# Optimization experiments

Measured on AMD Instinct MI355X. Metric: run time of the kernel, lower is better.

## Reference

```python
import jax, jax.numpy as jnp
import numpy as np

B, N, K, C, NH = 2, 16384, 16, 256, 4
HD = C // NH  # head_dim = 64


def knn_gather(feat, idx):
    # feat: [B, N, D], idx: [B, N, K] -> [B, N, K, D]
    b, n, k = idx.shape
    d = feat.shape[-1]
    flat = jnp.take_along_axis(feat, idx.reshape(b, n * k)[..., None], axis=1)
    return flat.reshape(b, n, k, d)


def setup_inputs() -> dict:
    key = jax.random.key(0)
    ks = jax.random.split(key, 16)
    s_c = 1.0 / np.sqrt(C)
    s_4 = 1.0 / np.sqrt(4.0)
    s_hd = 1.0 / np.sqrt(HD)
    return {
        'h': jax.random.normal(ks[0], (B, N, C), jnp.float32),
        'P': jax.random.normal(ks[1], (B, 3, N), jnp.float32),
        'idx': jax.random.randint(ks[2], (B, N, K), 0, N),
        'Wq': jax.random.normal(ks[3], (C, C), jnp.float32) * s_c,
        'Wk': jax.random.normal(ks[4], (C, C), jnp.float32) * s_c,
        'Wv': jax.random.normal(ks[5], (C, C), jnp.float32) * s_c,
        'Wp1': jax.random.normal(ks[6], (4, C), jnp.float32) * s_4,
        'bp1': jnp.zeros((C,), jnp.float32),
        'Wp2': jax.random.normal(ks[7], (C, C), jnp.float32) * s_c,
        'bp2': jnp.zeros((C,), jnp.float32),
        'Wa1': jax.random.normal(ks[8], (HD, HD), jnp.float32) * s_hd,
        'ba1': jnp.zeros((HD,), jnp.float32),
        'Wa2': jax.random.normal(ks[9], (HD, 1), jnp.float32) * s_hd,
        'ba2': jnp.zeros((1,), jnp.float32),
        'Wo': jax.random.normal(ks[10], (C, C), jnp.float32) * s_c,
        'bo': jnp.zeros((C,), jnp.float32),
    }


def reference(h, P, idx, Wq, Wk, Wv, Wp1, bp1, Wp2, bp2, Wa1, ba1, Wa2, ba2, Wo, bo):
    b, n, c = h.shape
    P_t = jnp.swapaxes(P, 1, 2)                       # [B, N, 3]
    P_nbr = knn_gather(P_t, idx)                      # [B, N, K, 3]
    rel_pos = P_nbr - P_t[:, :, None, :]              # [B, N, K, 3]
    dist = jnp.linalg.norm(rel_pos, axis=-1, keepdims=True)
    geom = jnp.concatenate([rel_pos, dist], axis=-1)  # [B, N, K, 4]
    pe = jax.nn.relu(geom @ Wp1 + bp1) @ Wp2 + bp2    # [B, N, K, C]
    pe = pe.reshape(b, n, K, NH, HD)

    Q = (h @ Wq).reshape(b, n, 1, NH, HD)
    K_nbr = knn_gather(h @ Wk, idx).reshape(b, n, K, NH, HD)
    V_nbr = knn_gather(h @ Wv, idx).reshape(b, n, K, NH, HD)

    relation = Q - K_nbr + pe                          # [B, N, K, NH, HD]
    logits = jax.nn.relu(relation @ Wa1 + ba1) @ Wa2 + ba2  # [B, N, K, NH, 1]
    attn = jax.nn.softmax(logits, axis=2)              # softmax over K
    agg = jnp.sum(attn * (V_nbr + pe), axis=2)         # [B, N, NH, HD]
    agg = agg.reshape(b, n, c)
    return agg @ Wo + bo
```

## Files before the change

kernel.cpp:

```cpp
#include <hip/hip_runtime.h>
#include <hip/hip_bf16.h>

#define BB 2
#define NN 16384
#define KK 16
#define CC 256
#define NHH 4
#define HDD 64
#define BN (BB*NN)
#define HP 260

typedef __attribute__((ext_vector_type(8))) short short8;
typedef __attribute__((ext_vector_type(4))) short s4;
typedef __attribute__((ext_vector_type(4))) float f32x4;

__device__ __forceinline__ float bf2f(unsigned short u) {
    union { unsigned u32; float f; } x; x.u32 = ((unsigned)u) << 16; return x.f;
}
__device__ __forceinline__ unsigned short f2bf(float f) {
    union { float f; unsigned u; } x; x.f = f;
    unsigned r = x.u + 0x7FFFu + ((x.u >> 16) & 1u);
    return (unsigned short)(r >> 16);
}
__device__ __forceinline__ short8 ld8_lds(const unsigned short* p) {
    s4 lo = *(const s4*)(p);
    s4 hi = *(const s4*)(p + 4);
    short8 r;
    r[0] = lo[0]; r[1] = lo[1]; r[2] = lo[2]; r[3] = lo[3];
    r[4] = hi[0]; r[5] = hi[1]; r[6] = hi[2]; r[7] = hi[3];
    return r;
}

__global__ __launch_bounds__(256) void prep_kernel(
    const float* __restrict__ Wq, const float* __restrict__ Wk,
    const float* __restrict__ Wv, const float* __restrict__ Wp2,
    const float* __restrict__ Wo, const float* __restrict__ Wa1,
    const float* __restrict__ bp2, const float* __restrict__ ba1,
    const float* __restrict__ Wp1,
    unsigned short* WqaT, unsigned short* WkaT, unsigned short* WvT,
    unsigned short* WpeaT, unsigned short* Wp2T, unsigned short* WoT,
    float* b_u, unsigned short* Wp1aT)
{
    const int z = blockIdx.y;
    const int t = threadIdx.x;
    if (z < 3) {
        const float* W = (z == 0) ? Wq : (z == 1) ? Wk : Wp2;
        unsigned short* out = (z == 0) ? WqaT : (z == 1) ? WkaT : WpeaT;
        const int k = blockIdx.x;
        __shared__ float wrow[CC];
        __shared__ float a1[HDD * HDD];
        wrow[t] = W[k * CC + t];
        for (int i = t; i < HDD * HDD; i += 256) a1[i] = Wa1[i];
        __syncthreads();
        const int c = t;
        const int h0 = c & ~63;
        const int cl = c & 63;
        float s = 0.f;
        #pragma unroll 8
        for (int j = 0; j < HDD; ++j) s += wrow[h0 + j] * a1[j * HDD + cl];
        out[c * CC + k] = f2bf(s);
    } else if (z < 6) {
        const float* W = (z == 3) ? Wv : (z == 4) ? Wp2 : Wo;
        unsigned short* out = (z == 3) ? WvT : (z == 4) ? Wp2T : WoT;
        const int k = blockIdx.x;
        out[t * CC + k] = f2bf(W[k * CC + t]);
    } else {
        if (blockIdx.x == 0) {
            __shared__ float a1[HDD * HDD];
            for (int i = t; i < HDD * HDD; i += 256) a1[i] = Wa1[i];
            __syncthreads();
            const int c = t;
            const int h0 = c & ~63;
            const int cl = c & 63;
            float s = ba1[cl];
            #pragma unroll 8
            for (int j = 0; j < HDD; ++j) s += bp2[h0 + j] * a1[j * HDD + cl];
            b_u[c] = s;
        } else if (blockIdx.x == 1) {
            const int c = t;
            #pragma unroll
            for (int j = 0; j < 8; ++j)
                Wp1aT[c * 8 + j] = (j < 4) ? f2bf(Wp1[j * CC + c]) : (unsigned short)0;
        }
    }
}

__global__ __launch_bounds__(256) void h2bf_kernel(const float* __restrict__ h,
                                                   unsigned short* __restrict__ hbf)
{
    const int i = blockIdx.x * blockDim.x + threadIdx.x;
    const float4 v = ((const float4*)h)[i];
    ushort4 o;
    o.x = f2bf(v.x); o.y = f2bf(v.y); o.z = f2bf(v.z); o.w = f2bf(v.w);
    ((ushort4*)hbf)[i] = o;
}

template<bool FINAL>
__global__ __launch_bounds__(256) void gemm64_kernel(
    const unsigned short* __restrict__ A,
    const unsigned short* __restrict__ BT0, const unsigned short* __restrict__ BT1,
    const unsigned short* __restrict__ BT2,
    unsigned short* D0, unsigned short* D1, unsigned short* D2,
    float* Dout, const float* __restrict__ bias)
{
    const int m0 = blockIdx.x * 64;
    const unsigned short* BT;
    unsigned short* Dst = nullptr;
    int z = 0;
    if (!FINAL) {
        z = blockIdx.y;
        BT  = (z == 0) ? BT0 : (z == 1) ? BT1 : BT2;
        Dst = (z == 0) ? D0  : (z == 1) ? D1  : D2;
    } else {
        BT = BT0;
    }

    __shared__ __align__(16) unsigned short As[64 * 264];
    const int t = threadIdx.x;
    #pragma unroll
    for (int i = 0; i < 8; ++i) {
        const int flat = i * 2048 + t * 8;
        const int r = flat >> 8, c = flat & 255;
        short8 v = *(const short8*)(A + (size_t)(m0 + r) * CC + c);
        *(short8*)(&As[r * 264 + c]) = v;
    }
    __syncthreads();

    const int lane = t & 63, w = t >> 6;
    const int lr = lane & 15, lg = lane >> 4;

    f32x4 acc[4][4];
    #pragma unroll
    for (int mi = 0; mi < 4; ++mi)
        #pragma unroll
        for (int ni = 0; ni < 4; ++ni) acc[mi][ni] = (f32x4){0.f, 0.f, 0.f, 0.f};

    #pragma unroll
    for (int kk = 0; kk < 8; ++kk) {
        const int ko = kk * 32 + lg * 8;
        short8 a[4];
        #pragma unroll
        for (int mi = 0; mi < 4; ++mi)
            a[mi] = *(const short8*)(&As[(mi * 16 + lr) * 264 + ko]);
        #pragma unroll
        for (int ni = 0; ni < 4; ++ni) {
            const int col = w * 64 + ni * 16 + lr;
            short8 b = *(const short8*)(BT + (size_t)col * CC + ko);
            #pragma unroll
            for (int mi = 0; mi < 4; ++mi)
                acc[mi][ni] = __builtin_amdgcn_mfma_f32_16x16x32_bf16(a[mi], b, acc[mi][ni], 0, 0, 0);
        }
    }

    #pragma unroll
    for (int mi = 0; mi < 4; ++mi) {
        #pragma unroll
        for (int ni = 0; ni < 4; ++ni) {
            const int col = w * 64 + ni * 16 + lr;
            const float bc = (FINAL || z == 0) ? bias[col] : 0.f;
            #pragma unroll
            for (int reg = 0; reg < 4; ++reg) {
                const int row = m0 + mi * 16 + lg * 4 + reg;
                const float v = acc[mi][ni][reg];
                if (FINAL) Dout[(size_t)row * CC + col] = v + bias[col];
                else       Dst[(size_t)row * CC + col] = f2bf(v + bc);
            }
        }
    }
}

__global__ __launch_bounds__(256, 3) void fused_attn_kernel(
    const float* __restrict__ P, const int* __restrict__ idx,
    const unsigned short* __restrict__ Wp1aT, const float* __restrict__ bp1,
    const float* __restrict__ Wa2, const float* __restrict__ bp2,
    const unsigned short* __restrict__ QAbf, const unsigned short* __restrict__ KAbf,
    const unsigned short* __restrict__ Vbf,  const unsigned short* __restrict__ WpeaT,
    const unsigned short* __restrict__ Wp2T,
    unsigned short* __restrict__ aggbf)
{
    const int pt0 = blockIdx.x * 4;
    const int b = pt0 >> 14;
    const int n0 = pt0 & (NN - 1);
    const int t = threadIdx.x;
    const int lane = t & 63, w = t >> 6;
    const int lr = lane & 15, lg = lane >> 4;

    __shared__ int nbrL[64];
    __shared__ __align__(16) unsigned short hidL[64 * HP];
    __shared__ __align__(16) unsigned short attnA[16 * 72];
    __shared__ unsigned short vbarL[16 * 72];

    const short8 zero8 = {0, 0, 0, 0, 0, 0, 0, 0};

    float qab[4][4];
    float wa2v[4];
    #pragma unroll
    for (int ni = 0; ni < 4; ++ni) {
        const int c = w * 64 + ni * 16 + lr;
        wa2v[ni] = Wa2[ni * 16 + lr];
        #pragma unroll
        for (int mi = 0; mi < 4; ++mi)
            qab[mi][ni] = bf2f(QAbf[(size_t)(pt0 + mi) * CC + c]);
    }

    for (int i = t; i < 576; i += 256) ((unsigned*)attnA)[i] = 0;

    float rx = 0.f, ry = 0.f, rz = 0.f, dd = 0.f;
    if (lane < 16) {
        const int nb_ = idx[(size_t)(pt0 + w) * KK + lane];
        nbrL[w * 16 + lane] = nb_;
        const float* Pb = P + (size_t)b * 3 * NN;
        const int nc = n0 + w;
        rx = Pb[nb_] - Pb[nc];
        ry = Pb[NN + nb_] - Pb[NN + nc];
        rz = Pb[2 * NN + nb_] - Pb[2 * NN + nc];
        dd = sqrtf(rx * rx + ry * ry + rz * rz);
    }
    short8 ag = zero8;
    if (lane < 16) {
        ag[0] = (short)f2bf(rx); ag[1] = (short)f2bf(ry);
        ag[2] = (short)f2bf(rz); ag[3] = (short)f2bf(dd);
    }
    #pragma unroll
    for (int nb = 0; nb < 16; ++nb) {
        short8 bb = (lg == 0) ? *(const short8*)(Wp1aT + (nb * 16 + lr) * 8) : zero8;
        const float bp = bp1[nb * 16 + lr];
        f32x4 ah = (f32x4){bp, bp, bp, bp};
        ah = __builtin_amdgcn_mfma_f32_16x16x32_bf16(ag, bb, ah, 0, 0, 0);
        #pragma unroll
        for (int reg = 0; reg < 4; ++reg)
            hidL[(w * 16 + lg * 4 + reg) * HP + nb * 16 + lr] = f2bf(fmaxf(ah[reg], 0.f));
    }
    __syncthreads();

    f32x4 acc[4][4];
    #pragma unroll
    for (int mi = 0; mi < 4; ++mi)
        #pragma unroll
        for (int ni = 0; ni < 4; ++ni) {
            const float v = qab[mi][ni];
            acc[mi][ni] = (f32x4){v, v, v, v};
        }

    #pragma unroll
    for (int kk = 0; kk < 8; ++kk) {
        const int ko = kk * 32 + lg * 8;
        short8 a[4];
        #pragma unroll
        for (int mi = 0; mi < 4; ++mi)
            a[mi] = ld8_lds(&hidL[(mi * 16 + lr) * HP + ko]);
        #pragma unroll
        for (int ni = 0; ni < 4; ++ni) {
            const int col = w * 64 + ni * 16 + lr;
            short8 bfr = *(const short8*)(WpeaT + (size_t)col * CC + ko);
            #pragma unroll
            for (int mi = 0; mi < 4; ++mi)
                acc[mi][ni] = __builtin_amdgcn_mfma_f32_16x16x32_bf16(a[mi], bfr, acc[mi][ni], 0, 0, 0);
        }
    }

    #pragma unroll
    for (int mi = 0; mi < 4; ++mi) {
        unsigned short ka[4][4];
        #pragma unroll
        for (int reg = 0; reg < 4; ++reg) {
            const int r = mi * 16 + lg * 4 + reg;
            const size_t base = ((size_t)b * NN + nbrL[r]) * CC;
            #pragma unroll
            for (int ni = 0; ni < 4; ++ni)
                ka[reg][ni] = KAbf[base + w * 64 + ni * 16 + lr];
        }
        float pl[4];
        #pragma unroll
        for (int reg = 0; reg < 4; ++reg) {
            float s = 0.f;
            #pragma unroll
            for (int ni = 0; ni < 4; ++ni) {
                const float u = acc[mi][ni][reg] - bf2f(ka[reg][ni]);
                s += fmaxf(u, 0.f) * wa2v[ni];
            }
            s += __shfl_xor(s, 1);
            s += __shfl_xor(s, 2);
            s += __shfl_xor(s, 4);
            s += __shfl_xor(s, 8);
            pl[reg] = s;
        }
        float m = fmaxf(fmaxf(pl[0], pl[1]), fmaxf(pl[2], pl[3]));
        m = fmaxf(m, __shfl_xor(m, 16));
        m = fmaxf(m, __shfl_xor(m, 32));
        float e[4], s = 0.f;
        #pragma unroll
        for (int reg = 0; reg < 4; ++reg) { e[reg] = __expf(pl[reg] - m); s += e[reg]; }
        s += __shfl_xor(s, 16);
        s += __shfl_xor(s, 32);
        const float inv = 1.f / s;
        if (lr == 0) {
            #pragma unroll
            for (int reg = 0; reg < 4; ++reg)
                attnA[(mi * 4 + w) * 72 + mi * 16 + lg * 4 + reg] = f2bf(e[reg] * inv);
        }
    }
    __syncthreads();

    const size_t bNN = (size_t)b * NN;
    ushort4 vv[16];
    #pragma unroll
    for (int k = 0; k < 16; ++k)
        vv[k] = *(const ushort4*)(Vbf + (bNN + nbrL[w * 16 + k]) * CC + lane * 4);

    #pragma unroll
    for (int ni = 0; ni < 4; ++ni) {
        const int colAbs = w * 64 + ni * 16 + lr;
        f32x4 ab = (f32x4){0.f, 0.f, 0.f, 0.f};
        #pragma unroll
        for (int kk = 0; kk < 2; ++kk) {
            short8 aa = ld8_lds(&attnA[lr * 72 + kk * 32 + lg * 8]);
            short8 hb;
            #pragma unroll
            for (int j = 0; j < 8; ++j)
                hb[j] = (short)hidL[(kk * 32 + lg * 8 + j) * HP + colAbs];
            ab = __builtin_amdgcn_mfma_f32_16x16x32_bf16(aa, hb, ab, 0, 0, 0);
        }
        #pragma unroll
        for (int reg = 0; reg < 4; ++reg)
            hidL[(lg * 4 + reg) * HP + colAbs] = f2bf(ab[reg]);
    }

    {
        const int hh = lane >> 4;
        const int dbase = (lane & 15) * 4;
        float s0 = 0.f, s1 = 0.f, s2 = 0.f, s3 = 0.f;
        #pragma unroll
        for (int k = 0; k < 16; ++k) {
            const float at = bf2f(attnA[(w * 4 + hh) * 72 + w * 16 + k]);
            s0 += at * bf2f((unsigned short)vv[k].x);
            s1 += at * bf2f((unsigned short)vv[k].y);
            s2 += at * bf2f((unsigned short)vv[k].z);
            s3 += at * bf2f((unsigned short)vv[k].w);
        }
        ushort4 o;
        o.x = f2bf(s0); o.y = f2bf(s1); o.z = f2bf(s2); o.w = f2bf(s3);
        *(ushort4*)(&vbarL[(w * 4 + hh) * 72 + dbase]) = o;
    }
    __syncthreads();

    f32x4 acc2[4];
    #pragma unroll
    for (int ni = 0; ni < 4; ++ni) acc2[ni] = (f32x4){0.f, 0.f, 0.f, 0.f};
    #pragma unroll
    for (int kk = 0; kk < 8; ++kk) {
        const int ko = kk * 32 + lg * 8;
        short8 a = ld8_lds(&hidL[lr * HP + ko]);
        #pragma unroll
        for (int ni = 0; ni < 4; ++ni) {
            const int col = w * 64 + ni * 16 + lr;
            short8 bfr = *(const short8*)(Wp2T + (size_t)col * CC + ko);
            acc2[ni] = __builtin_amdgcn_mfma_f32_16x16x32_bf16(a, bfr, acc2[ni], 0, 0, 0);
        }
    }
    #pragma unroll
    for (int ni = 0; ni < 4; ++ni) {
        const int cl = ni * 16 + lr;
        const int c = w * 64 + cl;
        float pv;
        if      (w == 0) pv = acc2[ni][0];
        else if (w == 1) pv = acc2[ni][1];
        else if (w == 2) pv = acc2[ni][2];
        else             pv = acc2[ni][3];
        const float v = pv + bf2f(vbarL[(lg * 4 + w) * 72 + cl]) + bp2[c];
        aggbf[(size_t)(pt0 + lg) * CC + c] = f2bf(v);
    }
}

extern "C" void kernel_launch(void* const* d_in, const int* in_sizes, int n_in,
                              void* d_out, int out_size, void* d_ws, size_t ws_size,
                              hipStream_t stream)
{
    const float* h   = (const float*)d_in[0];
    const float* P   = (const float*)d_in[1];
    const int*   idx = (const int*)d_in[2];
    const float* Wq  = (const float*)d_in[3];
    const float* Wk  = (const float*)d_in[4];
    const float* Wv  = (const float*)d_in[5];
    const float* Wp1 = (const float*)d_in[6];
    const float* bp1 = (const float*)d_in[7];
    const float* Wp2 = (const float*)d_in[8];
    const float* bp2 = (const float*)d_in[9];
    const float* Wa1 = (const float*)d_in[10];
    const float* ba1 = (const float*)d_in[11];
    const float* Wa2 = (const float*)d_in[12];
    const float* Wo  = (const float*)d_in[14];
    const float* bo  = (const float*)d_in[15];

    char* ws = (char*)d_ws;
    const size_t MB16 = 16777216;
    unsigned short* WqaT  = (unsigned short*)(ws + 0);
    unsigned short* WkaT  = (unsigned short*)(ws + 131072);
    unsigned short* WvT   = (unsigned short*)(ws + 262144);
    unsigned short* WpeaT = (unsigned short*)(ws + 393216);
    unsigned short* Wp2T  = (unsigned short*)(ws + 524288);
    unsigned short* WoT   = (unsigned short*)(ws + 655360);
    float*          b_u   = (float*)(ws + 786432);
    unsigned short* Wp1aT = (unsigned short*)(ws + 787456);
    const size_t base = 1 << 20;
    unsigned short* hbf   = (unsigned short*)(ws + base + 0 * MB16);
    unsigned short* QAbf  = (unsigned short*)(ws + base + 1 * MB16);
    unsigned short* KAbf  = (unsigned short*)(ws + base + 2 * MB16);
    unsigned short* Vbf   = (unsigned short*)(ws + base + 3 * MB16);
    unsigned short* aggbf = (unsigned short*)(ws + base + 4 * MB16);
    if (ws_size < base + 5 * MB16) return;

    prep_kernel<<<dim3(256, 7), 256, 0, stream>>>(Wq, Wk, Wv, Wp2, Wo, Wa1, bp2, ba1, Wp1,
                                                  WqaT, WkaT, WvT, WpeaT, Wp2T, WoT,
                                                  b_u, Wp1aT);
    h2bf_kernel<<<BN * CC / 4 / 256, 256, 0, stream>>>(h, hbf);
    gemm64_kernel<false><<<dim3(BN / 64, 3), 256, 0, stream>>>(
        hbf, WqaT, WkaT, WvT, QAbf, KAbf, Vbf, nullptr, b_u);
    fused_attn_kernel<<<BN / 4, 256, 0, stream>>>(P, idx, Wp1aT, bp1, Wa2, bp2,
                                                  QAbf, KAbf, Vbf, WpeaT, Wp2T, aggbf);
    gemm64_kernel<true><<<dim3(BN / 64, 1), 256, 0, stream>>>(
        aggbf, WoT, nullptr, nullptr, nullptr, nullptr, nullptr, (float*)d_out, bo);
}
```

Baseline: 442.0 us.

## Give each wave its own point so attention runs without block barriers

Each wave now computes the pe-attention GEMM for its own point's 16 neighbours across all 256 columns, rather than a column slice across all four points. The softmax and both weighted sums then stay within the wave, which removes two __syncthreads. The attention-weighted hidden sum moves from a sparse MFMA, whose attention tile was mostly zero-padded, to scalar FMAs into a separate hbarL buffer. The costs are higher register pressure (16 accumulators plus a 4x4 partial-logit array), a full 256-column pass over WpeaT per wave instead of a 64-column slice, and more LDS from the extra hbarL array.

```diff
diff --git a/kernel.cpp b/kernel.cpp
--- a/kernel.cpp
+++ b/kernel.cpp
@@ -187,23 +187,12 @@
 
     __shared__ int nbrL[64];
     __shared__ __align__(16) unsigned short hidL[64 * HP];
-    __shared__ __align__(16) unsigned short attnA[16 * 72];
+    __shared__ __align__(16) unsigned short hbarL[16 * HP];
+    __shared__ __align__(8)  unsigned short attnW[64 * 4];
     __shared__ unsigned short vbarL[16 * 72];
 
     const short8 zero8 = {0, 0, 0, 0, 0, 0, 0, 0};
-
-    float qab[4][4];
-    float wa2v[4];
-    #pragma unroll
-    for (int ni = 0; ni < 4; ++ni) {
-        const int c = w * 64 + ni * 16 + lr;
-        wa2v[ni] = Wa2[ni * 16 + lr];
-        #pragma unroll
-        for (int mi = 0; mi < 4; ++mi)
-            qab[mi][ni] = bf2f(QAbf[(size_t)(pt0 + mi) * CC + c]);
-    }
-
-    for (int i = t; i < 576; i += 256) ((unsigned*)attnA)[i] = 0;
+    const size_t bNN = (size_t)b * NN;
 
     float rx = 0.f, ry = 0.f, rz = 0.f, dd = 0.f;
     if (lane < 16) {
@@ -231,117 +220,133 @@
         for (int reg = 0; reg < 4; ++reg)
             hidL[(w * 16 + lg * 4 + reg) * HP + nb * 16 + lr] = f2bf(fmaxf(ah[reg], 0.f));
     }
-    __syncthreads();
-
-    f32x4 acc[4][4];
-    #pragma unroll
-    for (int mi = 0; mi < 4; ++mi)
-        #pragma unroll
-        for (int ni = 0; ni < 4; ++ni) {
-            const float v = qab[mi][ni];
-            acc[mi][ni] = (f32x4){v, v, v, v};
-        }
+
+    float wa2v[4];
+    #pragma unroll
+    for (int j = 0; j < 4; ++j) wa2v[j] = Wa2[j * 16 + lr];
+
+    f32x4 acc[16];
+    #pragma unroll
+    for (int ni = 0; ni < 16; ++ni) {
+        const float q = bf2f(QAbf[(size_t)(pt0 + w) * CC + ni * 16 + lr]);
+        acc[ni] = (f32x4){q, q, q, q};
+    }
 
     #pragma unroll
     for (int kk = 0; kk < 8; ++kk) {
         const int ko = kk * 32 + lg * 8;
-        short8 a[4];
-        #pragma unroll
-        for (int mi = 0; mi < 4; ++mi)
-            a[mi] = ld8_lds(&hidL[(mi * 16 + lr) * HP + ko]);
-        #pragma unroll
-        for (int ni = 0; ni < 4; ++ni) {
-            const int col = w * 64 + ni * 16 + lr;
-            short8 bfr = *(const short8*)(WpeaT + (size_t)col * CC + ko);
-            #pragma unroll
-            for (int mi = 0; mi < 4; ++mi)
-                acc[mi][ni] = __builtin_amdgcn_mfma_f32_16x16x32_bf16(a[mi], bfr, acc[mi][ni], 0, 0, 0);
-        }
-    }
-
-    #pragma unroll
-    for (int mi = 0; mi < 4; ++mi) {
-        unsigned short ka[4][4];
+        short8 a8 = ld8_lds(&hidL[(w * 16 + lr) * HP + ko]);
+        #pragma unroll
+        for (int ni = 0; ni < 16; ++ni) {
+            short8 b8 = *(const short8*)(WpeaT + (size_t)(ni * 16 + lr) * CC + ko);
+            acc[ni] = __builtin_amdgcn_mfma_f32_16x16x32_bf16(a8, b8, acc[ni], 0, 0, 0);
+        }
+    }
+
+    int nbq[4];
+    #pragma unroll
+    for (int reg = 0; reg < 4; ++reg) nbq[reg] = nbrL[w * 16 + lg * 4 + reg];
+
+    float pl[4][4];
+    #pragma unroll
+    for (int reg = 0; reg < 4; ++reg)
+        #pragma unroll
+        for (int h = 0; h < 4; ++h) pl[reg][h] = 0.f;
+
+    #pragma unroll
+    for (int ni = 0; ni < 16; ++ni) {
+        const int h = ni >> 2, wj = ni & 3;
         #pragma unroll
         for (int reg = 0; reg < 4; ++reg) {
-            const int r = mi * 16 + lg * 4 + reg;
-            const size_t base = ((size_t)b * NN + nbrL[r]) * CC;
-            #pragma unroll
-            for (int ni = 0; ni < 4; ++ni)
-                ka[reg][ni] = KAbf[base + w * 64 + ni * 16 + lr];
-        }
-        float pl[4];
-        #pragma unroll
-        for (int reg = 0; reg < 4; ++reg) {
-            float s = 0.f;
-            #pragma unroll
-            for (int ni = 0; ni < 4; ++ni) {
-                const float u = acc[mi][ni][reg] - bf2f(ka[reg][ni]);
-                s += fmaxf(u, 0.f) * wa2v[ni];
-            }
+            const unsigned short ka = KAbf[(bNN + nbq[reg]) * CC + ni * 16 + lr];
+            const float u = acc[ni][reg] - bf2f(ka);
+            pl[reg][h] += fmaxf(u, 0.f) * wa2v[wj];
+        }
+    }
+    #pragma unroll
+    for (int reg = 0; reg < 4; ++reg)
+        #pragma unroll
+        for (int h = 0; h < 4; ++h) {
+            float s = pl[reg][h];
             s += __shfl_xor(s, 1);
             s += __shfl_xor(s, 2);
             s += __shfl_xor(s, 4);
             s += __shfl_xor(s, 8);
-            pl[reg] = s;
-        }
-        float m = fmaxf(fmaxf(pl[0], pl[1]), fmaxf(pl[2], pl[3]));
+            pl[reg][h] = s;
+        }
+
+    float aval[4][4];
+    #pragma unroll
+    for (int h = 0; h < 4; ++h) {
+        float m = fmaxf(fmaxf(pl[0][h], pl[1][h]), fmaxf(pl[2][h], pl[3][h]));
         m = fmaxf(m, __shfl_xor(m, 16));
         m = fmaxf(m, __shfl_xor(m, 32));
         float e[4], s = 0.f;
         #pragma unroll
-        for (int reg = 0; reg < 4; ++reg) { e[reg] = __expf(pl[reg] - m); s += e[reg]; }
+        for (int reg = 0; reg < 4; ++reg) { e[reg] = __expf(pl[reg][h] - m); s += e[reg]; }
         s += __shfl_xor(s, 16);
         s += __shfl_xor(s, 32);
         const float inv = 1.f / s;
-        if (lr == 0) {
-            #pragma unroll
-            for (int reg = 0; reg < 4; ++reg)
-                attnA[(mi * 4 + w) * 72 + mi * 16 + lg * 4 + reg] = f2bf(e[reg] * inv);
-        }
-    }
-    __syncthreads();
-
-    const size_t bNN = (size_t)b * NN;
+        #pragma unroll
+        for (int reg = 0; reg < 4; ++reg) aval[reg][h] = e[reg] * inv;
+    }
+    if (lr < 4) {
+        #pragma unroll
+        for (int reg = 0; reg < 4; ++reg) {
+            const float v = (lr == 0) ? aval[reg][0] : (lr == 1) ? aval[reg][1]
+                          : (lr == 2) ? aval[reg][2] : aval[reg][3];
+            attnW[(w * 16 + lg * 4 + reg) * 4 + lr] = f2bf(v);
+        }
+    }
+
     ushort4 vv[16];
     #pragma unroll
     for (int k = 0; k < 16; ++k)
         vv[k] = *(const ushort4*)(Vbf + (bNN + nbrL[w * 16 + k]) * CC + lane * 4);
 
-    #pragma unroll
-    for (int ni = 0; ni < 4; ++ni) {
-        const int colAbs = w * 64 + ni * 16 + lr;
-        f32x4 ab = (f32x4){0.f, 0.f, 0.f, 0.f};
-        #pragma unroll
-        for (int kk = 0; kk < 2; ++kk) {
-            short8 aa = ld8_lds(&attnA[lr * 72 + kk * 32 + lg * 8]);
-            short8 hb;
+    {
+        float hp[4][4];
+        #pragma unroll
+        for (int h = 0; h < 4; ++h)
             #pragma unroll
-            for (int j = 0; j < 8; ++j)
-                hb[j] = (short)hidL[(kk * 32 + lg * 8 + j) * HP + colAbs];
-            ab = __builtin_amdgcn_mfma_f32_16x16x32_bf16(aa, hb, ab, 0, 0, 0);
-        }
-        #pragma unroll
-        for (int reg = 0; reg < 4; ++reg)
-            hidL[(lg * 4 + reg) * HP + colAbs] = f2bf(ab[reg]);
+            for (int j = 0; j < 4; ++j) hp[h][j] = 0.f;
+        #pragma unroll
+        for (int k = 0; k < 16; ++k) {
+            const ushort4 hraw = *(const ushort4*)(&hidL[(w * 16 + k) * HP + lane * 4]);
+            const ushort4 araw = *(const ushort4*)(&attnW[(w * 16 + k) * 4]);
+            const float f0 = bf2f(hraw.x), f1 = bf2f(hraw.y), f2 = bf2f(hraw.z), f3 = bf2f(hraw.w);
+            const float a0 = bf2f(araw.x), a1 = bf2f(araw.y), a2 = bf2f(araw.z), a3 = bf2f(araw.w);
+            hp[0][0] += a0 * f0; hp[0][1] += a0 * f1; hp[0][2] += a0 * f2; hp[0][3] += a0 * f3;
+            hp[1][0] += a1 * f0; hp[1][1] += a1 * f1; hp[1][2] += a1 * f2; hp[1][3] += a1 * f3;
+            hp[2][0] += a2 * f0; hp[2][1] += a2 * f1; hp[2][2] += a2 * f2; hp[2][3] += a2 * f3;
+            hp[3][0] += a3 * f0; hp[3][1] += a3 * f1; hp[3][2] += a3 * f2; hp[3][3] += a3 * f3;
+        }
+        #pragma unroll
+        for (int h = 0; h < 4; ++h) {
+            ushort4 o;
+            o.x = f2bf(hp[h][0]); o.y = f2bf(hp[h][1]);
+            o.z = f2bf(hp[h][2]); o.w = f2bf(hp[h][3]);
+            *(ushort4*)(&hbarL[(w * 4 + h) * HP + lane * 4]) = o;
+        }
     }
 
     {
-        const int hh = lane >> 4;
-        const int dbase = (lane & 15) * 4;
-        float s0 = 0.f, s1 = 0.f, s2 = 0.f, s3 = 0.f;
+        float vp[4] = {0.f, 0.f, 0.f, 0.f};
         #pragma unroll
         for (int k = 0; k < 16; ++k) {
-            const float at = bf2f(attnA[(w * 4 + hh) * 72 + w * 16 + k]);
-            s0 += at * bf2f((unsigned short)vv[k].x);
-            s1 += at * bf2f((unsigned short)vv[k].y);
-            s2 += at * bf2f((unsigned short)vv[k].z);
-            s3 += at * bf2f((unsigned short)vv[k].w);
+            const ushort4 araw = *(const ushort4*)(&attnW[(w * 16 + k) * 4]);
+            const float a = (lg == 0) ? bf2f(araw.x) : (lg == 1) ? bf2f(araw.y)
+                          : (lg == 2) ? bf2f(araw.z) : bf2f(araw.w);
+            vp[0] += a * bf2f(vv[k].x);
+            vp[1] += a * bf2f(vv[k].y);
+            vp[2] += a * bf2f(vv[k].z);
+            vp[3] += a * bf2f(vv[k].w);
         }
         ushort4 o;
-        o.x = f2bf(s0); o.y = f2bf(s1); o.z = f2bf(s2); o.w = f2bf(s3);
-        *(ushort4*)(&vbarL[(w * 4 + hh) * 72 + dbase]) = o;
-    }
+        o.x = f2bf(vp[0]); o.y = f2bf(vp[1]); o.z = f2bf(vp[2]); o.w = f2bf(vp[3]);
+        *(ushort4*)(&vbarL[(w * 4 + lg) * 72 + (lane & 15) * 4]) = o;
+    }
+
     __syncthreads();
 
     f32x4 acc2[4];
@@ -350,7 +355,7 @@
     #pragma unroll
     for (int kk = 0; kk < 8; ++kk) {
         const int ko = kk * 32 + lg * 8;
-        short8 a = ld8_lds(&hidL[lr * HP + ko]);
+        short8 a = ld8_lds(&hbarL[lr * HP + ko]);
         #pragma unroll
         for (int ni = 0; ni < 4; ++ni) {
             const int col = w * 64 + ni * 16 + lr;
```

Measured after the change: 939.8 us. 113% more time.
